# Optimization experiments

Hardware: AMD Instinct MI355X
Metric: run time of the kernel (lower is better)

## Reference

```python
import jax, jax.numpy as jnp
import numpy as np

H, W = 256, 256
DX, DY = 1.0, 1.0
EI, KC, GC = 1.0, 1.0, 1.0
LAYERS = [2, 256, 512, 1024, H * W]
B = 64


def _d2x(f, dx):
    # reflect-pad width 1 on x (last axis), stencil [1, -2, 1]
    p = jnp.pad(f, ((0, 0), (0, 0), (0, 0), (1, 1)), mode='reflect')
    return (p[..., :-2] - 2.0 * p[..., 1:-1] + p[..., 2:]) / (dx * dx)


def _d2y(f, dy):
    p = jnp.pad(f, ((0, 0), (0, 0), (1, 1), (0, 0)), mode='reflect')
    return (p[:, :, :-2, :] - 2.0 * p[:, :, 1:-1, :] + p[:, :, 2:, :]) / (dy * dy)


def setup_inputs() -> dict:
    key = jax.random.key(0)
    ks = jax.random.split(key, 10)
    inp = {
        'x_coloc': jax.random.normal(ks[0], (B, LAYERS[0]), jnp.float32),
        'P': jax.random.normal(ks[1], (B, H * W), jnp.float32),
    }
    for i in range(4):
        inp[f'W{i + 1}'] = jax.random.normal(ks[2 + i], (LAYERS[i], LAYERS[i + 1]), jnp.float32) / np.sqrt(LAYERS[i]).astype(np.float32)
        inp[f'b{i + 1}'] = jnp.zeros((LAYERS[i + 1],), jnp.float32)
    return inp


def reference(x_coloc, P, W1, b1, W2, b2, W3, b3, W4, b4):
    # MLP field predictor: Linear+ReLU x3, final Linear -> [B, H*W]
    h = jax.nn.relu(x_coloc @ W1 + b1)
    h = jax.nn.relu(h @ W2 + b2)
    h = jax.nn.relu(h @ W3 + b3)
    f = h @ W4 + b4                      # [B, H*W]
    fm = f.reshape(B, 1, H, W)

    fx2 = _d2x(fm, DX)                   # d2/dx2
    fy2 = _d2y(fm, DY)                   # d2/dy2
    lap = fx2 + fy2
    biharmonic = _d2x(lap, DX) + _d2y(lap, DY)

    residual = EI * biharmonic + GC * (fx2 + fy2) + KC * fm - P.reshape(B, 1, H, W)
    return residual.reshape(B, H * W)
```

## Files before the change

### kernel.cpp

```cpp
#include <hip/hip_runtime.h>


#define BATCH 64
#define NPIX 65536

typedef __attribute__((ext_vector_type(8))) short short8_t;
typedef __attribute__((ext_vector_type(4))) float f32x4;

#define LDS_FENCE()   asm volatile("s_waitcnt lgkmcnt(0)" ::: "memory")
#define MEM_ORDER()   asm volatile("" ::: "memory")

__device__ __forceinline__ short f2bf(float x) {
    unsigned u = __float_as_uint(x);
    unsigned r = (u + 0x7fffu + ((u >> 16) & 1u)) >> 16;
    return (short)r;
}

__global__ void k_layer12(const float* __restrict__ x, const float* __restrict__ W1,
                          const float* __restrict__ b1, const float* __restrict__ W2,
                          const float* __restrict__ b2, float* __restrict__ h2) {
    __shared__ float As[16][64];
    __shared__ float Ws[64][16];
    int tid = threadIdx.x;
    int tn = tid & 15, tm = tid >> 4;
    int n0 = blockIdx.x * 16, m0 = blockIdx.y * 16;
    float acc = 0.f;
    for (int k0 = 0; k0 < 256; k0 += 64) {
#pragma unroll
        for (int j = 0; j < 4; ++j) {
            int e = j * 256 + tid;
            int m = m0 + (e >> 6), kk = k0 + (e & 63);
            float v = x[m * 2 + 0] * W1[kk] + x[m * 2 + 1] * W1[256 + kk] + b1[kk];
            As[e >> 6][e & 63] = v > 0.f ? v : 0.f;
        }
#pragma unroll
        for (int j = 0; j < 4; ++j) {
            int e = j * 256 + tid;
            Ws[e >> 4][e & 15] = W2[(k0 + (e >> 4)) * 512 + n0 + (e & 15)];
        }
        __syncthreads();
#pragma unroll
        for (int k = 0; k < 64; ++k)
            acc += As[tm][k] * Ws[k][tn];
        __syncthreads();
    }
    acc += b2[n0 + tn];
    acc = acc > 0.f ? acc : 0.f;
    h2[(m0 + tm) * 512 + n0 + tn] = acc;
}

__global__ void k_layer3(const float* __restrict__ A, const float* __restrict__ Wt,
                         const float* __restrict__ bias, short* __restrict__ out_bf) {
    __shared__ float As[16][64];
    __shared__ float Ws[64][16];
    int tid = threadIdx.x;
    int tn = tid & 15, tm = tid >> 4;
    int n0 = blockIdx.x * 16, m0 = blockIdx.y * 16;
    float acc = 0.f;
    for (int k0 = 0; k0 < 512; k0 += 64) {
#pragma unroll
        for (int j = 0; j < 4; ++j) {
            int e = j * 256 + tid;
            As[e >> 6][e & 63] = A[(m0 + (e >> 6)) * 512 + k0 + (e & 63)];
        }
#pragma unroll
        for (int j = 0; j < 4; ++j) {
            int e = j * 256 + tid;
            Ws[e >> 4][e & 15] = Wt[(k0 + (e >> 4)) * 1024 + n0 + (e & 15)];
        }
        __syncthreads();
#pragma unroll
        for (int k = 0; k < 64; ++k)
            acc += As[tm][k] * Ws[k][tn];
        __syncthreads();
    }
    acc += bias[n0 + tn];
    acc = acc > 0.f ? acc : 0.f;
    out_bf[(m0 + tm) * 1024 + n0 + tn] = f2bf(acc);
}

__global__ __launch_bounds__(64) void k_gemm_mfma(
        const short* __restrict__ A,
        const float* __restrict__ W,
        const float* __restrict__ bias,
        float* __restrict__ f) {
    __shared__ float Bl[32 * 64];
    const int lane = threadIdx.x;
    const int lr = lane & 15;
    const int g = lane >> 4;
    const int n0w = blockIdx.x * 64;

    f32x4 acc[4][4];
#pragma unroll
    for (int a = 0; a < 4; ++a)
#pragma unroll
        for (int b = 0; b < 4; ++b)
            acc[a][b] = {0.f, 0.f, 0.f, 0.f};

    const short* ap = A + lr * 1024 + g * 8;

    f32x4 R[8];
    auto gload = [&](int k0) {
#pragma unroll
        for (int i = 0; i < 8; ++i) {
            int k = i * 4 + (lane >> 4);
            R[i] = *(const f32x4*)(W + (size_t)(k0 + k) * NPIX + n0w + (lane & 15) * 4);
        }
    };
    auto lwrite = [&]() {
#pragma unroll
        for (int i = 0; i < 8; ++i) {
            int k = i * 4 + (lane >> 4);
            int cc = ((lane & 15) * 4) ^ (((i >> 1) & 3) << 4);
            *(f32x4*)&Bl[k * 64 + cc] = R[i];
        }
    };

    short8_t aC[4], aN[4];

    gload(0);
#pragma unroll
    for (int mt = 0; mt < 4; ++mt)
        aC[mt] = *(const short8_t*)(ap + mt * 16384);
    lwrite();
    gload(32);
#pragma unroll
    for (int mt = 0; mt < 4; ++mt)
        aN[mt] = *(const short8_t*)(ap + mt * 16384 + 32);
    LDS_FENCE();

    for (int s = 0; s < 32; ++s) {
#pragma unroll
        for (int t = 0; t < 4; ++t) {
            const int csw = (t * 16 + lr) ^ (g << 4);
            short8_t bf;
#pragma unroll
            for (int j = 0; j < 8; ++j)
                bf[j] = f2bf(Bl[(g * 8 + j) * 64 + csw]);
#pragma unroll
            for (int mt = 0; mt < 4; ++mt)
                acc[mt][t] = __builtin_amdgcn_mfma_f32_16x16x32_bf16(aC[mt], bf, acc[mt][t], 0, 0, 0);
        }
        MEM_ORDER();
        if (s < 31) {
            lwrite();
            LDS_FENCE();
            if (s < 30) gload((s + 2) * 32);
#pragma unroll
            for (int mt = 0; mt < 4; ++mt) aC[mt] = aN[mt];
            if (s < 30) {
#pragma unroll
                for (int mt = 0; mt < 4; ++mt)
                    aN[mt] = *(const short8_t*)(ap + mt * 16384 + (s + 2) * 32);
            }
        }
    }

#pragma unroll
    for (int h = 0; h < 2; ++h) {
        MEM_ORDER();
#pragma unroll
        for (int mtl = 0; mtl < 2; ++mtl) {
            int mt = h * 2 + mtl;
#pragma unroll
            for (int t = 0; t < 4; ++t) {
                float bb = bias[n0w + t * 16 + lr];
#pragma unroll
                for (int r = 0; r < 4; ++r)
                    Bl[(mtl * 16 + g * 4 + r) * 64 + t * 16 + lr] = acc[mt][t][r] + bb;
            }
        }
        LDS_FENCE();
#pragma unroll
        for (int jj = 0; jj < 8; ++jj) {
            int rl = jj * 4 + (lane >> 4);
            f32x4 v = *(const f32x4*)&Bl[rl * 64 + (lane & 15) * 4];
            *(f32x4*)(f + (size_t)(h * 32 + rl) * NPIX + n0w + (lane & 15) * 4) = v;
        }
        MEM_ORDER();
    }
}

#define ROWS 16
__device__ __forceinline__ int rfl(int i) {
    return i < 0 ? -i : (i > 255 ? 510 - i : i);
}
__global__ void k_stencil(const float* __restrict__ f, const float* __restrict__ P,
                          float* __restrict__ out) {
    __shared__ float fs[ROWS + 4][256];
    int x = threadIdx.x;
    int y0 = blockIdx.x * ROWS;
    int b = blockIdx.y;
    const float* fb = f + (size_t)b * NPIX;
    for (int t = 0; t < ROWS + 4; ++t) {
        int gy = rfl(y0 - 2 + t);
        fs[t][x] = fb[gy * 256 + x];
    }
    __syncthreads();

    int xm = x == 0 ? 1 : x - 1;
    int xp = x == 255 ? 254 : x + 1;

    auto lapAt = [&](int j, int i) {
        int s = j - y0 + 2;
        int sm = rfl(j - 1) - y0 + 2;
        int sp = rfl(j + 1) - y0 + 2;
        int im = i == 0 ? 1 : i - 1;
        int ip = i == 255 ? 254 : i + 1;
        float c = fs[s][i];
        return (fs[sm][i] - 2.f * c + fs[sp][i]) + (fs[s][im] - 2.f * c + fs[s][ip]);
    };

    for (int r = 0; r < ROWS; ++r) {
        int y = y0 + r;
        float lc = lapAt(y, x);
        float lym = lapAt(rfl(y - 1), x);
        float lyp = lapAt(rfl(y + 1), x);
        float lxm = lapAt(y, xm);
        float lxp = lapAt(y, xp);
        float bih = (lym - 2.f * lc + lyp) + (lxm - 2.f * lc + lxp);
        float fc = fs[r + 2][x];
        size_t idx = (size_t)b * NPIX + y * 256 + x;
        out[idx] = bih + lc + fc - P[idx];
    }
}

extern "C" void kernel_launch(void* const* d_in, const int* in_sizes, int n_in,
                              void* d_out, int out_size, void* d_ws, size_t ws_size,
                              hipStream_t stream) {
    const float* x  = (const float*)d_in[0];
    const float* P  = (const float*)d_in[1];
    const float* W1 = (const float*)d_in[2];
    const float* b1 = (const float*)d_in[3];
    const float* W2 = (const float*)d_in[4];
    const float* b2 = (const float*)d_in[5];
    const float* W3 = (const float*)d_in[6];
    const float* b3 = (const float*)d_in[7];
    const float* W4 = (const float*)d_in[8];
    const float* b4 = (const float*)d_in[9];
    float* out = (float*)d_out;

    char* ws = (char*)d_ws;
    float* h2  = (float*)(ws);
    short* h3b = (short*)(ws + (128 << 10));
    float* f   = (float*)(ws + (256 << 10));

    k_layer12<<<dim3(512 / 16, 4), 256, 0, stream>>>(x, W1, b1, W2, b2, h2);
    k_layer3<<<dim3(1024 / 16, 4), 256, 0, stream>>>(h2, W3, b3, h3b);
    k_gemm_mfma<<<NPIX / 64, 64, 0, stream>>>(h3b, W4, b4, f);
    k_stencil<<<dim3(256 / ROWS, BATCH), 256, 0, stream>>>(f, P, out);
}
```

Baseline: 93.20 us.

## Restructure final GEMM with 4-wave blocks and async global-to-LDS double buffering

Rewrites the large W4 GEMM kernel to use 256-thread blocks covering 128 output columns, with each wave owning 32 columns. W4 and activation tiles stream straight into double-buffered LDS through global_load_lds, using swizzled layouts and vmcnt waits plus barriers to overlap loads with MFMA work. The activation tile is now shared across waves through LDS instead of being reloaded per wave from registers. The epilogue drops LDS staging and writes results directly to global memory with scalar stores, which may be less coalesced.

```diff
diff --git a/kernel.cpp b/kernel.cpp
--- a/kernel.cpp
+++ b/kernel.cpp
@@ -6,9 +6,6 @@
 
 typedef __attribute__((ext_vector_type(8))) short short8_t;
 typedef __attribute__((ext_vector_type(4))) float f32x4;
-
-#define LDS_FENCE()   asm volatile("s_waitcnt lgkmcnt(0)" ::: "memory")
-#define MEM_ORDER()   asm volatile("" ::: "memory")
 
 __device__ __forceinline__ short f2bf(float x) {
     unsigned u = __float_as_uint(x);
@@ -79,105 +76,98 @@
     out_bf[(m0 + tm) * 1024 + n0 + tn] = f2bf(acc);
 }
 
-__global__ __launch_bounds__(64) void k_gemm_mfma(
+__global__ __launch_bounds__(256) void k_gemm_mfma(
         const short* __restrict__ A,
         const float* __restrict__ W,
         const float* __restrict__ bias,
         float* __restrict__ f) {
-    __shared__ float Bl[32 * 64];
-    const int lane = threadIdx.x;
+    __shared__ float Wt[2][32 * 128];
+    __shared__ short At[2][4 * 64 * 8];
+    const int tid = threadIdx.x;
+    const int w = tid >> 6;
+    const int lane = tid & 63;
     const int lr = lane & 15;
     const int g = lane >> 4;
-    const int n0w = blockIdx.x * 64;
-
-    f32x4 acc[4][4];
+    const int n0 = blockIdx.x * 128;
+
+    f32x4 acc[4][2];
 #pragma unroll
     for (int a = 0; a < 4; ++a)
 #pragma unroll
-        for (int b = 0; b < 4; ++b)
+        for (int b = 0; b < 2; ++b)
             acc[a][b] = {0.f, 0.f, 0.f, 0.f};
 
-    const short* ap = A + lr * 1024 + g * 8;
-
-    f32x4 R[8];
-    auto gload = [&](int k0) {
-#pragma unroll
-        for (int i = 0; i < 8; ++i) {
-            int k = i * 4 + (lane >> 4);
-            R[i] = *(const f32x4*)(W + (size_t)(k0 + k) * NPIX + n0w + (lane & 15) * 4);
+    auto stage = [&](int b, int s) {
+#pragma unroll
+        for (int i = 0; i < 4; ++i) {
+            int c = i * 256 + tid;
+            int k = c >> 5;
+            int q4 = (c & 31) * 4;
+            int csw = q4 ^ (((k >> 3) & 1) << 4);
+            const float* src = W + (size_t)(s * 32 + k) * NPIX + n0 + csw;
+            __builtin_amdgcn_global_load_lds(
+                (const __attribute__((address_space(1))) void*)src,
+                (__attribute__((address_space(3))) void*)((char*)&Wt[b][0] + c * 16),
+                16, 0, 0);
+        }
+        {
+            int kq = tid >> 6;
+            int ms = tid & 63;
+            int md = ms ^ (kq << 2);
+            const short* asrc = A + md * 1024 + s * 32 + kq * 8;
+            __builtin_amdgcn_global_load_lds(
+                (const __attribute__((address_space(1))) void*)asrc,
+                (__attribute__((address_space(3))) void*)((char*)&At[b][0] + tid * 16),
+                16, 0, 0);
         }
     };
-    auto lwrite = [&]() {
-#pragma unroll
-        for (int i = 0; i < 8; ++i) {
-            int k = i * 4 + (lane >> 4);
-            int cc = ((lane & 15) * 4) ^ (((i >> 1) & 3) << 4);
-            *(f32x4*)&Bl[k * 64 + cc] = R[i];
-        }
-    };
-
-    short8_t aC[4], aN[4];
-
-    gload(0);
-#pragma unroll
-    for (int mt = 0; mt < 4; ++mt)
-        aC[mt] = *(const short8_t*)(ap + mt * 16384);
-    lwrite();
-    gload(32);
-#pragma unroll
-    for (int mt = 0; mt < 4; ++mt)
-        aN[mt] = *(const short8_t*)(ap + mt * 16384 + 32);
-    LDS_FENCE();
+
+    stage(0, 0);
 
     for (int s = 0; s < 32; ++s) {
-#pragma unroll
-        for (int t = 0; t < 4; ++t) {
-            const int csw = (t * 16 + lr) ^ (g << 4);
-            short8_t bf;
+        const int cur = s & 1;
+        if (s < 31) {
+            stage(cur ^ 1, s + 1);
+            asm volatile("s_waitcnt vmcnt(5)" ::: "memory");
+        } else {
+            asm volatile("s_waitcnt vmcnt(0)" ::: "memory");
+        }
+        __builtin_amdgcn_sched_barrier(0);
+        __builtin_amdgcn_s_barrier();
+
+        short8_t afr[4];
+#pragma unroll
+        for (int mt = 0; mt < 4; ++mt) {
+            int mrow = mt * 16 + lr;
+            afr[mt] = *(const short8_t*)((const short*)&At[cur][0] +
+                                         g * 512 + (mrow ^ (g << 2)) * 8);
+        }
+#pragma unroll
+        for (int t = 0; t < 2; ++t) {
+            const int col = w * 32 + t * 16 + lr;
+            const int csw = col ^ ((g & 1) << 4);
+            short8_t bfr;
 #pragma unroll
             for (int j = 0; j < 8; ++j)
-                bf[j] = f2bf(Bl[(g * 8 + j) * 64 + csw]);
+                bfr[j] = f2bf(Wt[cur][(g * 8 + j) * 128 + csw]);
 #pragma unroll
             for (int mt = 0; mt < 4; ++mt)
-                acc[mt][t] = __builtin_amdgcn_mfma_f32_16x16x32_bf16(aC[mt], bf, acc[mt][t], 0, 0, 0);
-        }
-        MEM_ORDER();
-        if (s < 31) {
-            lwrite();
-            LDS_FENCE();
-            if (s < 30) gload((s + 2) * 32);
-#pragma unroll
-            for (int mt = 0; mt < 4; ++mt) aC[mt] = aN[mt];
-            if (s < 30) {
-#pragma unroll
-                for (int mt = 0; mt < 4; ++mt)
-                    aN[mt] = *(const short8_t*)(ap + mt * 16384 + (s + 2) * 32);
-            }
-        }
-    }
-
-#pragma unroll
-    for (int h = 0; h < 2; ++h) {
-        MEM_ORDER();
-#pragma unroll
-        for (int mtl = 0; mtl < 2; ++mtl) {
-            int mt = h * 2 + mtl;
-#pragma unroll
-            for (int t = 0; t < 4; ++t) {
-                float bb = bias[n0w + t * 16 + lr];
-#pragma unroll
-                for (int r = 0; r < 4; ++r)
-                    Bl[(mtl * 16 + g * 4 + r) * 64 + t * 16 + lr] = acc[mt][t][r] + bb;
-            }
-        }
-        LDS_FENCE();
-#pragma unroll
-        for (int jj = 0; jj < 8; ++jj) {
-            int rl = jj * 4 + (lane >> 4);
-            f32x4 v = *(const f32x4*)&Bl[rl * 64 + (lane & 15) * 4];
-            *(f32x4*)(f + (size_t)(h * 32 + rl) * NPIX + n0w + (lane & 15) * 4) = v;
-        }
-        MEM_ORDER();
+                acc[mt][t] = __builtin_amdgcn_mfma_f32_16x16x32_bf16(afr[mt], bfr, acc[mt][t], 0, 0, 0);
+        }
+        __builtin_amdgcn_s_barrier();
+    }
+
+#pragma unroll
+    for (int t = 0; t < 2; ++t) {
+        const int col = n0 + w * 32 + t * 16 + lr;
+        float bb = bias[col];
+#pragma unroll
+        for (int mt = 0; mt < 4; ++mt) {
+            int rowb = mt * 16 + g * 4;
+#pragma unroll
+            for (int r = 0; r < 4; ++r)
+                f[(size_t)(rowb + r) * NPIX + col] = acc[mt][t][r] + bb;
+        }
     }
 }
 
@@ -247,6 +237,6 @@
 
     k_layer12<<<dim3(512 / 16, 4), 256, 0, stream>>>(x, W1, b1, W2, b2, h2);
     k_layer3<<<dim3(1024 / 16, 4), 256, 0, stream>>>(h2, W3, b3, h3b);
-    k_gemm_mfma<<<NPIX / 64, 64, 0, stream>>>(h3b, W4, b4, f);
+    k_gemm_mfma<<<NPIX / 128, 256, 0, stream>>>(h3b, W4, b4, f);
     k_stencil<<<dim3(256 / ROWS, BATCH), 256, 0, stream>>>(f, P, out);
 }
```

After: 87.39 us. 6.2% less time.
